# Performance work log

Measured on AMD Instinct MI355X. Metric: run time of the kernel, lower is better.

## Reference

```python
import jax, jax.numpy as jnp
import numpy as np

# Config (mirrors init_kwargs)
IN_FEATURES = 1024
N_CLASSES = 50257
CUTOFFS = [4000, 20000, 50257]   # cutoffs + [n_classes]
SHORTLIST = 4000
N_CLUSTERS = 2
HEAD_SIZE = SHORTLIST + N_CLUSTERS  # 4002
HSZ = [IN_FEATURES // 4, IN_FEATURES // 16]   # div_value**1, div_value**2 -> 256, 64
OSZ = [CUTOFFS[1] - CUTOFFS[0], CUTOFFS[2] - CUTOFFS[1]]  # 16000, 30257
N = 4096


def setup_inputs() -> dict:
    key = jax.random.key(0)
    ks = jax.random.split(key, 8)
    s = 0.02
    return {
        "myinput": jax.random.normal(ks[0], (N, IN_FEATURES), dtype=jnp.float32),
        "target": jax.random.randint(ks[1], (N,), 0, N_CLASSES),
        # head Linear (bias=False): weight stored as [in, out]
        "head_W": (jax.random.normal(ks[2], (IN_FEATURES, HEAD_SIZE), dtype=jnp.float32) * s),
        # tail cluster 0: Linear(in, 256, bias=False) -> Linear(256, 16000, bias=False)
        "t0_W1": (jax.random.normal(ks[3], (IN_FEATURES, HSZ[0]), dtype=jnp.float32) * s),
        "t0_W2": (jax.random.normal(ks[4], (HSZ[0], OSZ[0]), dtype=jnp.float32) * s),
        # tail cluster 1: Linear(in, 64, bias=False) -> Linear(64, 30257, bias=False)
        "t1_W1": (jax.random.normal(ks[5], (IN_FEATURES, HSZ[1]), dtype=jnp.float32) * s),
        "t1_W2": (jax.random.normal(ks[6], (HSZ[1], OSZ[1]), dtype=jnp.float32) * s),
    }


def _cluster_logprob(x, target, W1, W2, lo, hi, mask):
    # low-rank tail projection for one cluster, computed densely over all rows
    # then masked by membership (same math as the torch gather/scatter dispatch).
    logits = (x @ W1) @ W2                       # [N, osz]
    rel = jnp.clip(target - lo, 0, hi - lo - 1)  # in-range dummy for non-members
    picked = jnp.take_along_axis(logits, rel[:, None], axis=1)[:, 0]
    lp = picked - jax.nn.logsumexp(logits, axis=1)  # log_softmax gathered at rel
    return jnp.where(mask, lp, jnp.float32(0.0))


def reference(myinput, target, head_W, t0_W1, t0_W2, t1_W1, t1_W2):
    # Dropout (tail_drop) is identity in eval mode.
    in0 = (target >= CUTOFFS[0]) & (target < CUTOFFS[1])
    in1 = target >= CUTOFFS[1]
    # gather index into head: raw target for shortlist, cluster token otherwise
    gather_inds = jnp.where(in0, SHORTLIST, jnp.where(in1, SHORTLIST + 1, target))
    head_lp = jax.nn.log_softmax(myinput @ head_W, axis=-1)   # [N, 4002]
    out = jnp.take_along_axis(head_lp, gather_inds[:, None], axis=1)[:, 0]
    out = out + _cluster_logprob(myinput, target, t0_W1, t0_W2, CUTOFFS[0], CUTOFFS[1], in0)
    out = out + _cluster_logprob(myinput, target, t1_W1, t1_W2, CUTOFFS[1], CUTOFFS[2], in1)
    loss = -jnp.mean(out)
    return out, loss
```

## Files before the change

kernel.cpp:

```cpp
#include <hip/hip_runtime.h>
#include <hip/hip_bf16.h>
#include <math.h>
#include <stdint.h>

#define N_ROWS 4096
#define IN_F   1024
#define HEAD_N 4002
#define C0_H   256
#define C0_N   16000
#define C1_H   64
#define C1_N   30257
#define CUT0   4000
#define CUT1   20000
#define HW1    384

#define LOG2E 1.4426950408889634f
#define LN2   0.6931471805599453f

typedef __attribute__((ext_vector_type(8))) short bf16x8;
typedef __attribute__((ext_vector_type(4))) float f32x4;

__device__ __forceinline__ float exp2_fast(float x) {
    return __builtin_amdgcn_exp2f(x);
}

__device__ __forceinline__ ushort f2bf(float f) {
    uint32_t u = __builtin_bit_cast(uint32_t, f);
    uint32_t r = (u + 0x7fffu + ((u >> 16) & 1u)) >> 16;
    return (ushort)r;
}
__device__ __forceinline__ float bf2f(ushort u) {
    return __builtin_bit_cast(float, (uint32_t)u << 16);
}

__device__ __forceinline__ void gload_lds_16(const void* gsrc, void* ldst) {
    __builtin_amdgcn_global_load_lds(
        (const __attribute__((address_space(1))) void*)(uintptr_t)gsrc,
        (__attribute__((address_space(3))) void*)(uint32_t)(uintptr_t)ldst,
        16, 0, 0);
}

__global__ __launch_bounds__(256)
void cast_f32_bf16(const float* __restrict__ in, ushort* __restrict__ out, int n)
{
    int i = (blockIdx.x * 256 + threadIdx.x) * 4;
    if (i >= n) return;
    float4 v = *reinterpret_cast<const float4*>(in + i);
    ushort4 o;
    o.x = f2bf(v.x); o.y = f2bf(v.y); o.z = f2bf(v.z); o.w = f2bf(v.w);
    *reinterpret_cast<ushort4*>(out + i) = o;
}

__global__ __launch_bounds__(256)
void castT(const float* __restrict__ B, ushort* __restrict__ BT, int K, int N,
           float scale)
{
    __shared__ float t[32][33];
    const int tx = threadIdx.x, ty = threadIdx.y;
    const int n0 = blockIdx.x * 32, k0 = blockIdx.y * 32;
    #pragma unroll
    for (int i = 0; i < 4; ++i) {
        int n = n0 + tx;
        t[ty + i * 8][tx] = (n < N) ? B[(size_t)(k0 + ty + i * 8) * N + n] : 0.0f;
    }
    __syncthreads();
    #pragma unroll
    for (int i = 0; i < 4; ++i) {
        int n = n0 + ty + i * 8;
        BT[(size_t)n * K + k0 + tx] = f2bf(t[tx][ty + i * 8] * scale);
    }
}

__global__ __launch_bounds__(256)
void gemm_out(const ushort* __restrict__ A, int lda,
              const ushort* __restrict__ BT, int ldb, int K,
              int Nreal, ushort* __restrict__ Cout, int ldc)
{
    __shared__ ushort As[128 * 32];
    __shared__ ushort Bs[128 * 32];
    const int tid = threadIdx.x;
    const int l = tid & 63, w = tid >> 6;
    const int rowBase = blockIdx.y * 128, colBase = blockIdx.x * 128;
    const int rsel = l & 15, ksel = l >> 4;
    const int sr = l >> 2, skq = (l & 3) * 8;

    f32x4 acc[2][8];
    #pragma unroll
    for (int mi = 0; mi < 2; ++mi)
        #pragma unroll
        for (int ni = 0; ni < 8; ++ni) acc[mi][ni] = (f32x4){0.f, 0.f, 0.f, 0.f};

    for (int k0 = 0; k0 < K; k0 += 32) {
        #pragma unroll
        for (int i = 0; i < 2; ++i) {
            const int c = w + i * 4;
            gload_lds_16(A + (size_t)(rowBase + c * 16 + sr) * lda + k0 + skq,
                         (char*)As + c * 1024);
            gload_lds_16(BT + (size_t)(colBase + c * 16 + sr) * ldb + k0 + skq,
                         (char*)Bs + c * 1024);
        }
        __syncthreads();
        bf16x8 af[2], bfr[8];
        #pragma unroll
        for (int mi = 0; mi < 2; ++mi)
            af[mi] = *reinterpret_cast<const bf16x8*>(As + (w * 32 + mi * 16 + rsel) * 32 + ksel * 8);
        #pragma unroll
        for (int ni = 0; ni < 8; ++ni)
            bfr[ni] = *reinterpret_cast<const bf16x8*>(Bs + (ni * 16 + rsel) * 32 + ksel * 8);
        #pragma unroll
        for (int mi = 0; mi < 2; ++mi)
            #pragma unroll
            for (int ni = 0; ni < 8; ++ni)
                acc[mi][ni] = __builtin_amdgcn_mfma_f32_16x16x32_bf16(af[mi], bfr[ni], acc[mi][ni], 0, 0, 0);
        __syncthreads();
    }
    #pragma unroll
    for (int mi = 0; mi < 2; ++mi)
        #pragma unroll
        for (int ni = 0; ni < 8; ++ni) {
            const int col = colBase + ni * 16 + rsel;
            if (col < Nreal) {
                #pragma unroll
                for (int j = 0; j < 4; ++j) {
                    const int row = rowBase + w * 32 + mi * 16 + ksel * 4 + j;
                    Cout[(size_t)row * ldc + col] = f2bf(acc[mi][ni][j]);
                }
            }
        }
}

__global__ __launch_bounds__(256, 2)
void sumexp_pipe(const ushort* __restrict__ A, int lda,
                 const ushort* __restrict__ BT, int ldb,
                 int K, int nCT, int ntiles, int Nreal,
                 float* __restrict__ ps, int nsplit)
{
    __shared__ ushort As[2][128 * 32];
    __shared__ ushort Bs[2][256 * 32];
    __shared__ float sred[128];

    const int id = blockIdx.x;
    const int xsplit = ((id >> 8) << 3) + (id & 7);
    const int yrow   = (id & 255) >> 3;

    const int tid = threadIdx.x;
    const int l = tid & 63, w = tid >> 6;
    const int rowBase = yrow * 128;
    const int rsel = l & 15, ksel = l >> 4;

    const int kchunks = K >> 5;
    const int ct0 = xsplit * ntiles;
    const int ctn = min(ntiles, nCT - ct0);
    const int nch = ctn * kchunks;

    const int srow = l >> 2;
    const int skq = ((((l & 3) << 4) ^ ((srow & 3) << 4)) >> 1);

    const int wrow = (w >> 1) * 64;
    const int wcol = (w & 1) * 128;
    const int koff = (ksel * 8) ^ ((rsel & 3) << 3);

    f32x4 acc[4][8];
    float s_run[4][4];
    #pragma unroll
    for (int mi = 0; mi < 4; ++mi)
        #pragma unroll
        for (int j = 0; j < 4; ++j) s_run[mi][j] = 0.f;

    int i_kh = 0, i_ct = 0, issued = 0;
    #define ISSUE()                                                            \
    do {                                                                       \
        const int buf = issued & 1;                                            \
        const int k0 = i_kh << 5;                                              \
        const size_t cb = (size_t)(ct0 + i_ct) << 8;                           \
        _Pragma("unroll")                                                      \
        for (int i = 0; i < 2; ++i) {      \
            const int c = w * 2 + i;                                           \
            gload_lds_16(A + (size_t)(rowBase + c * 16 + srow) * lda + k0 + skq,\
                         (char*)&As[buf][0] + c * 1024);                       \
        }                                                                      \
        _Pragma("unroll")                                                      \
        for (int i = 0; i < 4; ++i) {    \
            const int c = w * 4 + i;                                           \
            gload_lds_16(BT + (cb + c * 16 + srow) * ldb + k0 + skq,           \
                         (char*)&Bs[buf][0] + c * 1024);                       \
        }                                                                      \
        ++issued;                                                              \
        if (++i_kh == kchunks) { i_kh = 0; ++i_ct; }                           \
    } while (0)

    ISSUE();
    if (nch > 1) ISSUE();

    int c_kh = 0;
    int c_colBase = ct0 << 8;

    for (int ch = 0; ch < nch; ++ch) {
        if (ch + 1 < nch) asm volatile("s_waitcnt vmcnt(6)" ::: "memory");
        else              asm volatile("s_waitcnt vmcnt(0)" ::: "memory");
        __builtin_amdgcn_s_barrier();

        if (c_kh == 0) {
            #pragma unroll
            for (int mi = 0; mi < 4; ++mi)
                #pragma unroll
                for (int ni = 0; ni < 8; ++ni)
                    acc[mi][ni] = (f32x4){0.f, 0.f, 0.f, 0.f};
        }

        const int buf = ch & 1;
        bf16x8 af[4], bfr[8];
        #pragma unroll
        for (int mi = 0; mi < 4; ++mi)
            af[mi] = *reinterpret_cast<const bf16x8*>(
                &As[buf][(wrow + mi * 16 + rsel) * 32 + koff]);
        #pragma unroll
        for (int ni = 0; ni < 8; ++ni)
            bfr[ni] = *reinterpret_cast<const bf16x8*>(
                &Bs[buf][(wcol + ni * 16 + rsel) * 32 + koff]);
        #pragma unroll
        for (int mi = 0; mi < 4; ++mi)
            #pragma unroll
            for (int ni = 0; ni < 8; ++ni)
                acc[mi][ni] = __builtin_amdgcn_mfma_f32_16x16x32_bf16(
                    af[mi], bfr[ni], acc[mi][ni], 0, 0, 0);

        __builtin_amdgcn_s_barrier();
        if (issued < nch) ISSUE();

        if (c_kh == kchunks - 1) {
            const int cbase = c_colBase + wcol;
            if (cbase + 128 > Nreal) {
                #pragma unroll
                for (int ni = 0; ni < 8; ++ni) {
                    const bool ok = (cbase + ni * 16 + rsel) < Nreal;
                    #pragma unroll
                    for (int mi = 0; mi < 4; ++mi)
                        #pragma unroll
                        for (int j = 0; j < 4; ++j)
                            s_run[mi][j] += ok ? exp2_fast(acc[mi][ni][j]) : 0.f;
                }
            } else {
                #pragma unroll
                for (int mi = 0; mi < 4; ++mi)
                    #pragma unroll
                    for (int ni = 0; ni < 8; ++ni)
                        #pragma unroll
                        for (int j = 0; j < 4; ++j)
                            s_run[mi][j] += exp2_fast(acc[mi][ni][j]);
            }
            c_kh = 0;
            c_colBase += 256;
        } else {
            ++c_kh;
        }
    }
    #undef ISSUE

    #pragma unroll
    for (int mi = 0; mi < 4; ++mi)
        #pragma unroll
        for (int j = 0; j < 4; ++j) {
            float S = s_run[mi][j];
            #pragma unroll
            for (int off = 8; off; off >>= 1) S += __shfl_xor(S, off);
            s_run[mi][j] = S;
            if ((w & 1) == 1 && rsel == 0)
                sred[wrow + mi * 16 + ksel * 4 + j] = S;
        }
    __syncthreads();
    if ((w & 1) == 0 && rsel == 0) {
        #pragma unroll
        for (int mi = 0; mi < 4; ++mi)
            #pragma unroll
            for (int j = 0; j < 4; ++j) {
                const int lrow = wrow + mi * 16 + ksel * 4 + j;
                ps[(size_t)(rowBase + lrow) * nsplit + xsplit] =
                    s_run[mi][j] + sred[lrow];
            }
    }
}

__global__ __launch_bounds__(256)
void gather_dot(const ushort* __restrict__ x_bf,
                const ushort* __restrict__ h_comb,
                const ushort* __restrict__ headWT,
                const ushort* __restrict__ t0W2T,
                const ushort* __restrict__ t1W2T,
                const int* __restrict__ target,
                float* __restrict__ pk_h, float* __restrict__ pk_c)
{
    const int r = blockIdx.x * 4 + (threadIdx.x >> 6);
    const int l = threadIdx.x & 63;
    const int t = target[r];

    const int gh = (t < CUT0) ? t : ((t < CUT1) ? CUT0 : CUT0 + 1);
    const ushort* xr = x_bf + (size_t)r * IN_F + l * 16;
    const ushort* wr = headWT + (size_t)gh * IN_F + l * 16;
    float s = 0.f;
    #pragma unroll
    for (int v = 0; v < 2; ++v) {
        ushort4 xa = *reinterpret_cast<const ushort4*>(xr + v * 8);
        ushort4 xb = *reinterpret_cast<const ushort4*>(xr + v * 8 + 4);
        ushort4 wa = *reinterpret_cast<const ushort4*>(wr + v * 8);
        ushort4 wb = *reinterpret_cast<const ushort4*>(wr + v * 8 + 4);
        s += bf2f(xa.x) * bf2f(wa.x) + bf2f(xa.y) * bf2f(wa.y)
           + bf2f(xa.z) * bf2f(wa.z) + bf2f(xa.w) * bf2f(wa.w)
           + bf2f(xb.x) * bf2f(wb.x) + bf2f(xb.y) * bf2f(wb.y)
           + bf2f(xb.z) * bf2f(wb.z) + bf2f(xb.w) * bf2f(wb.w);
    }
    #pragma unroll
    for (int off = 32; off; off >>= 1) s += __shfl_xor(s, off);
    if (l == 0) pk_h[r] = s * LN2;

    if (t >= CUT0) {
        float c = 0.f;
        if (t < CUT1) {
            const ushort* hr = h_comb + (size_t)r * HW1 + l * 4;
            const ushort* vr = t0W2T + (size_t)(t - CUT0) * C0_H + l * 4;
            ushort4 ha = *reinterpret_cast<const ushort4*>(hr);
            ushort4 va = *reinterpret_cast<const ushort4*>(vr);
            c = bf2f(ha.x) * bf2f(va.x) + bf2f(ha.y) * bf2f(va.y)
              + bf2f(ha.z) * bf2f(va.z) + bf2f(ha.w) * bf2f(va.w);
        } else {
            c = bf2f(h_comb[(size_t)r * HW1 + C0_H + l]) *
                bf2f(t1W2T[(size_t)(t - CUT1) * C1_H + l]);
        }
        #pragma unroll
        for (int off = 32; off; off >>= 1) c += __shfl_xor(c, off);
        if (l == 0) pk_c[r] = c * LN2;
    }
}

__global__ __launch_bounds__(256)
void combine_rows(const float* __restrict__ ps_h, const float* __restrict__ ps_0,
                  const float* __restrict__ ps_1,
                  const float* __restrict__ pk_h, const float* __restrict__ pk_c,
                  const int* __restrict__ target, float* __restrict__ out,
                  int ns_h, int ns_0, int ns_1)
{
    const int r = blockIdx.x * 256 + threadIdx.x;
    if (r >= N_ROWS) return;
    float S = 0.f;
    const float* p = ps_h + (size_t)r * ns_h;
    for (int i = 0; i < ns_h; ++i) S += p[i];
    float o = pk_h[r] - __logf(S);
    const int t = target[r];
    if (t >= CUT0) {
        const float* q; int n;
        if (t < CUT1) { q = ps_0 + (size_t)r * ns_0; n = ns_0; }
        else          { q = ps_1 + (size_t)r * ns_1; n = ns_1; }
        float S2 = 0.f;
        for (int i = 0; i < n; ++i) S2 += q[i];
        o += pk_c[r] - __logf(S2);
    }
    out[r] = o;
}

__global__ __launch_bounds__(256)
void finalize_loss(const float* __restrict__ out, float* __restrict__ loss)
{
    float s = 0.f;
    for (int r = threadIdx.x; r < N_ROWS; r += 256) s += out[r];
    #pragma unroll
    for (int off = 32; off; off >>= 1) s += __shfl_xor(s, off);
    __shared__ float red[4];
    if ((threadIdx.x & 63) == 0) red[threadIdx.x >> 6] = s;
    __syncthreads();
    if (threadIdx.x == 0)
        loss[0] = -(red[0] + red[1] + red[2] + red[3]) / (float)N_ROWS;
}

extern "C" void kernel_launch(void* const* d_in, const int* in_sizes, int n_in,
                              void* d_out, int out_size, void* d_ws, size_t ws_size,
                              hipStream_t stream)
{
    const float* x      = (const float*)d_in[0];
    const int*   target = (const int*)  d_in[1];
    const float* head_W = (const float*)d_in[2];
    const float* t0_W1  = (const float*)d_in[3];
    const float* t0_W2  = (const float*)d_in[4];
    const float* t1_W1  = (const float*)d_in[5];
    const float* t1_W2  = (const float*)d_in[6];
    float* out = (float*)d_out;

    const int HPAD  = 4096;
    const int C0PAD = 16128;
    const int C1PAD = 30464;
    const int nCT_h = HPAD / 256;
    const int nCT_0 = C0PAD / 256;
    const int nCT_1 = C1PAD / 256;

    const int NT_H = 2,  NS_H = 8;
    const int NT_0 = 4,  NS_0 = 16;
    const int NT_1 = 5,  NS_1 = 24;

    ushort* us = (ushort*)d_ws;
    ushort* x_bf   = us; us += (size_t)N_ROWS * IN_F;
    ushort* headWT = us; us += (size_t)HPAD * IN_F;
    ushort* hW1T   = us; us += (size_t)HW1 * IN_F;
    ushort* t0W2T  = us; us += (size_t)C0PAD * C0_H;
    ushort* t1W2T  = us; us += (size_t)C1PAD * C1_H;
    ushort* h_comb = us; us += (size_t)N_ROWS * HW1;

    float* ws   = (float*)us;
    float* ps_h = ws; ws += (size_t)N_ROWS * NS_H;
    float* ps_0 = ws; ws += (size_t)N_ROWS * NS_0;
    float* ps_1 = ws; ws += (size_t)N_ROWS * NS_1;
    float* pk_h = ws; ws += N_ROWS;
    float* pk_c = ws; ws += N_ROWS;

    const dim3 blk(256);

    hipLaunchKernelGGL(cast_f32_bf16, dim3(N_ROWS * IN_F / 1024), blk, 0, stream,
                       x, x_bf, N_ROWS * IN_F);
    hipLaunchKernelGGL(castT, dim3(HPAD / 32, IN_F / 32), dim3(32, 8), 0, stream,
                       head_W, headWT, IN_F, HEAD_N, LOG2E);
    hipLaunchKernelGGL(castT, dim3(C0_H / 32, IN_F / 32), dim3(32, 8), 0, stream,
                       t0_W1, hW1T, IN_F, C0_H, 1.0f);
    hipLaunchKernelGGL(castT, dim3(128 / 32, IN_F / 32), dim3(32, 8), 0, stream,
                       t1_W1, hW1T + (size_t)C0_H * IN_F, IN_F, C1_H, 1.0f);
    hipLaunchKernelGGL(castT, dim3(C0PAD / 32, C0_H / 32), dim3(32, 8), 0, stream,
                       t0_W2, t0W2T, C0_H, C0_N, LOG2E);
    hipLaunchKernelGGL(castT, dim3(C1PAD / 32, C1_H / 32), dim3(32, 8), 0, stream,
                       t1_W2, t1W2T, C1_H, C1_N, LOG2E);

    hipLaunchKernelGGL(gemm_out, dim3(HW1 / 128, N_ROWS / 128), blk, 0, stream,
                       x_bf, IN_F, hW1T, IN_F, IN_F, C0_H + C1_H, h_comb, HW1);

    hipLaunchKernelGGL(sumexp_pipe, dim3(NS_H * 32), blk, 0, stream,
                       x_bf, IN_F, headWT, IN_F, IN_F, nCT_h, NT_H, HEAD_N, ps_h, NS_H);
    hipLaunchKernelGGL(sumexp_pipe, dim3(NS_0 * 32), blk, 0, stream,
                       h_comb, HW1, t0W2T, C0_H, C0_H, nCT_0, NT_0, C0_N, ps_0, NS_0);
    hipLaunchKernelGGL(sumexp_pipe, dim3(NS_1 * 32), blk, 0, stream,
                       h_comb + C0_H, HW1, t1W2T, C1_H, C1_H, nCT_1, NT_1, C1_N, ps_1, NS_1);

    hipLaunchKernelGGL(gather_dot, dim3(N_ROWS / 4), blk, 0, stream,
                       x_bf, h_comb, headWT, t0W2T, t1W2T, target, pk_h, pk_c);
    hipLaunchKernelGGL(combine_rows, dim3(N_ROWS / 256), blk, 0, stream,
                       ps_h, ps_0, ps_1, pk_h, pk_c, target, out, NS_H, NS_0, NS_1);
    hipLaunchKernelGGL(finalize_loss, dim3(1), blk, 0, stream, out, out + N_ROWS);
}
```

Before: 197.1 us.

## Reshape sumexp tiles to 256 rows by 128 cols and drop cross-wave reduction

The fused GEMM+sum-exp kernel now uses a 256x128 block tile instead of 128x256. Each wave owns 64 full rows across all 128 columns, so per-row partial sums come straight from a shuffle reduction and the LDS cross-wave reduction and its barrier go away. Split counts and tiles per split are retuned, occupancy is raised to 3 blocks per SM, and blocks with no work are guarded. In exchange, every wave re-reads the whole B tile from LDS, and the extra splits enlarge the partial-sum buffer that combine_rows must reduce.

```diff
diff --git a/kernel.cpp b/kernel.cpp
--- a/kernel.cpp
+++ b/kernel.cpp
@@ -129,35 +129,32 @@
         }
 }
 
-__global__ __launch_bounds__(256, 2)
+__global__ __launch_bounds__(256, 3)
 void sumexp_pipe(const ushort* __restrict__ A, int lda,
                  const ushort* __restrict__ BT, int ldb,
                  int K, int nCT, int ntiles, int Nreal,
                  float* __restrict__ ps, int nsplit)
 {
-    __shared__ ushort As[2][128 * 32];
-    __shared__ ushort Bs[2][256 * 32];
-    __shared__ float sred[128];
+    __shared__ ushort As[2][256 * 32];
+    __shared__ ushort Bs[2][128 * 32];
 
     const int id = blockIdx.x;
-    const int xsplit = ((id >> 8) << 3) + (id & 7);
-    const int yrow   = (id & 255) >> 3;
+    const int xsplit = ((id >> 7) << 3) + (id & 7);
+    const int yrow   = (id >> 3) & 15;
 
     const int tid = threadIdx.x;
     const int l = tid & 63, w = tid >> 6;
-    const int rowBase = yrow * 128;
+    const int rowBase = yrow * 256;
     const int rsel = l & 15, ksel = l >> 4;
 
     const int kchunks = K >> 5;
     const int ct0 = xsplit * ntiles;
     const int ctn = min(ntiles, nCT - ct0);
-    const int nch = ctn * kchunks;
+    const int nch = (ctn > 0) ? ctn * kchunks : 0;
 
     const int srow = l >> 2;
     const int skq = ((((l & 3) << 4) ^ ((srow & 3) << 4)) >> 1);
 
-    const int wrow = (w >> 1) * 64;
-    const int wcol = (w & 1) * 128;
     const int koff = (ksel * 8) ^ ((rsel & 3) << 3);
 
     f32x4 acc[4][8];
@@ -172,16 +169,16 @@
     do {                                                                       \
         const int buf = issued & 1;                                            \
         const int k0 = i_kh << 5;                                              \
-        const size_t cb = (size_t)(ct0 + i_ct) << 8;                           \
+        const size_t cb = (size_t)(ct0 + i_ct) << 7;                           \
         _Pragma("unroll")                                                      \
-        for (int i = 0; i < 2; ++i) {      \
-            const int c = w * 2 + i;                                           \
+        for (int i = 0; i < 4; ++i) {    \
+            const int c = w * 4 + i;                                           \
             gload_lds_16(A + (size_t)(rowBase + c * 16 + srow) * lda + k0 + skq,\
                          (char*)&As[buf][0] + c * 1024);                       \
         }                                                                      \
         _Pragma("unroll")                                                      \
-        for (int i = 0; i < 4; ++i) {    \
-            const int c = w * 4 + i;                                           \
+        for (int i = 0; i < 2; ++i) {      \
+            const int c = w * 2 + i;                                           \
             gload_lds_16(BT + (cb + c * 16 + srow) * ldb + k0 + skq,           \
                          (char*)&Bs[buf][0] + c * 1024);                       \
         }                                                                      \
@@ -189,70 +186,71 @@
         if (++i_kh == kchunks) { i_kh = 0; ++i_ct; }                           \
     } while (0)
 
-    ISSUE();
-    if (nch > 1) ISSUE();
-
-    int c_kh = 0;
-    int c_colBase = ct0 << 8;
-
-    for (int ch = 0; ch < nch; ++ch) {
-        if (ch + 1 < nch) asm volatile("s_waitcnt vmcnt(6)" ::: "memory");
-        else              asm volatile("s_waitcnt vmcnt(0)" ::: "memory");
-        __builtin_amdgcn_s_barrier();
-
-        if (c_kh == 0) {
+    if (nch > 0) {
+        ISSUE();
+        if (nch > 1) ISSUE();
+
+        int c_kh = 0;
+        int c_colBase = ct0 << 7;
+
+        for (int ch = 0; ch < nch; ++ch) {
+            if (ch + 1 < nch) asm volatile("s_waitcnt vmcnt(6)" ::: "memory");
+            else              asm volatile("s_waitcnt vmcnt(0)" ::: "memory");
+            __builtin_amdgcn_s_barrier();
+
+            if (c_kh == 0) {
+                #pragma unroll
+                for (int mi = 0; mi < 4; ++mi)
+                    #pragma unroll
+                    for (int ni = 0; ni < 8; ++ni)
+                        acc[mi][ni] = (f32x4){0.f, 0.f, 0.f, 0.f};
+            }
+
+            const int buf = ch & 1;
+            bf16x8 af[4], bfr[8];
+            #pragma unroll
+            for (int mi = 0; mi < 4; ++mi)
+                af[mi] = *reinterpret_cast<const bf16x8*>(
+                    &As[buf][(w * 64 + mi * 16 + rsel) * 32 + koff]);
+            #pragma unroll
+            for (int ni = 0; ni < 8; ++ni)
+                bfr[ni] = *reinterpret_cast<const bf16x8*>(
+                    &Bs[buf][(ni * 16 + rsel) * 32 + koff]);
             #pragma unroll
             for (int mi = 0; mi < 4; ++mi)
                 #pragma unroll
                 for (int ni = 0; ni < 8; ++ni)
-                    acc[mi][ni] = (f32x4){0.f, 0.f, 0.f, 0.f};
-        }
-
-        const int buf = ch & 1;
-        bf16x8 af[4], bfr[8];
-        #pragma unroll
-        for (int mi = 0; mi < 4; ++mi)
-            af[mi] = *reinterpret_cast<const bf16x8*>(
-                &As[buf][(wrow + mi * 16 + rsel) * 32 + koff]);
-        #pragma unroll
-        for (int ni = 0; ni < 8; ++ni)
-            bfr[ni] = *reinterpret_cast<const bf16x8*>(
-                &Bs[buf][(wcol + ni * 16 + rsel) * 32 + koff]);
-        #pragma unroll
-        for (int mi = 0; mi < 4; ++mi)
-            #pragma unroll
-            for (int ni = 0; ni < 8; ++ni)
-                acc[mi][ni] = __builtin_amdgcn_mfma_f32_16x16x32_bf16(
-                    af[mi], bfr[ni], acc[mi][ni], 0, 0, 0);
-
-        __builtin_amdgcn_s_barrier();
-        if (issued < nch) ISSUE();
-
-        if (c_kh == kchunks - 1) {
-            const int cbase = c_colBase + wcol;
-            if (cbase + 128 > Nreal) {
-                #pragma unroll
-                for (int ni = 0; ni < 8; ++ni) {
-                    const bool ok = (cbase + ni * 16 + rsel) < Nreal;
+                    acc[mi][ni] = __builtin_amdgcn_mfma_f32_16x16x32_bf16(
+                        af[mi], bfr[ni], acc[mi][ni], 0, 0, 0);
+
+            __builtin_amdgcn_s_barrier();
+            if (issued < nch) ISSUE();
+
+            if (c_kh == kchunks - 1) {
+                if (c_colBase + 128 > Nreal) {
+                    #pragma unroll
+                    for (int ni = 0; ni < 8; ++ni) {
+                        const bool ok = (c_colBase + ni * 16 + rsel) < Nreal;
+                        #pragma unroll
+                        for (int mi = 0; mi < 4; ++mi)
+                            #pragma unroll
+                            for (int j = 0; j < 4; ++j)
+                                s_run[mi][j] += ok ? exp2_fast(acc[mi][ni][j]) : 0.f;
+                    }
+                } else {
                     #pragma unroll
                     for (int mi = 0; mi < 4; ++mi)
                         #pragma unroll
-                        for (int j = 0; j < 4; ++j)
-                            s_run[mi][j] += ok ? exp2_fast(acc[mi][ni][j]) : 0.f;
+                        for (int ni = 0; ni < 8; ++ni)
+                            #pragma unroll
+                            for (int j = 0; j < 4; ++j)
+                                s_run[mi][j] += exp2_fast(acc[mi][ni][j]);
                 }
+                c_kh = 0;
+                c_colBase += 128;
             } else {
-                #pragma unroll
-                for (int mi = 0; mi < 4; ++mi)
-                    #pragma unroll
-                    for (int ni = 0; ni < 8; ++ni)
-                        #pragma unroll
-                        for (int j = 0; j < 4; ++j)
-                            s_run[mi][j] += exp2_fast(acc[mi][ni][j]);
+                ++c_kh;
             }
-            c_kh = 0;
-            c_colBase += 256;
-        } else {
-            ++c_kh;
         }
     }
     #undef ISSUE
@@ -264,21 +262,11 @@
             float S = s_run[mi][j];
             #pragma unroll
             for (int off = 8; off; off >>= 1) S += __shfl_xor(S, off);
-            s_run[mi][j] = S;
-            if ((w & 1) == 1 && rsel == 0)
-                sred[wrow + mi * 16 + ksel * 4 + j] = S;
+            if (rsel == 0) {
+                const int row = rowBase + w * 64 + mi * 16 + ksel * 4 + j;
+                ps[(size_t)row * nsplit + xsplit] = S;
+            }
         }
-    __syncthreads();
-    if ((w & 1) == 0 && rsel == 0) {
-        #pragma unroll
-        for (int mi = 0; mi < 4; ++mi)
-            #pragma unroll
-            for (int j = 0; j < 4; ++j) {
-                const int lrow = wrow + mi * 16 + ksel * 4 + j;
-                ps[(size_t)(rowBase + lrow) * nsplit + xsplit] =
-                    s_run[mi][j] + sred[lrow];
-            }
-    }
 }
 
 __global__ __launch_bounds__(256)
@@ -387,13 +375,13 @@
     const int HPAD  = 4096;
     const int C0PAD = 16128;
     const int C1PAD = 30464;
-    const int nCT_h = HPAD / 256;
-    const int nCT_0 = C0PAD / 256;
-    const int nCT_1 = C1PAD / 256;
-
-    const int NT_H = 2,  NS_H = 8;
-    const int NT_0 = 4,  NS_0 = 16;
-    const int NT_1 = 5,  NS_1 = 24;
+    const int nCT_h = HPAD / 128;
+    const int nCT_0 = C0PAD / 128;
+    const int nCT_1 = C1PAD / 128;
+
+    const int NT_H = 2,  NS_H = 16;
+    const int NT_0 = 3,  NS_0 = 48;
+    const int NT_1 = 5,  NS_1 = 48;
 
     ushort* us = (ushort*)d_ws;
     ushort* x_bf   = us; us += (size_t)N_ROWS * IN_F;
@@ -428,11 +416,11 @@
     hipLaunchKernelGGL(gemm_out, dim3(HW1 / 128, N_ROWS / 128), blk, 0, stream,
                        x_bf, IN_F, hW1T, IN_F, IN_F, C0_H + C1_H, h_comb, HW1);
 
-    hipLaunchKernelGGL(sumexp_pipe, dim3(NS_H * 32), blk, 0, stream,
+    hipLaunchKernelGGL(sumexp_pipe, dim3(NS_H * 16), blk, 0, stream,
                        x_bf, IN_F, headWT, IN_F, IN_F, nCT_h, NT_H, HEAD_N, ps_h, NS_H);
-    hipLaunchKernelGGL(sumexp_pipe, dim3(NS_0 * 32), blk, 0, stream,
+    hipLaunchKernelGGL(sumexp_pipe, dim3(NS_0 * 16), blk, 0, stream,
                        h_comb, HW1, t0W2T, C0_H, C0_H, nCT_0, NT_0, C0_N, ps_0, NS_0);
-    hipLaunchKernelGGL(sumexp_pipe, dim3(NS_1 * 32), blk, 0, stream,
+    hipLaunchKernelGGL(sumexp_pipe, dim3(NS_1 * 16), blk, 0, stream,
                        h_comb + C0_H, HW1, t1W2T, C1_H, C1_H, nCT_1, NT_1, C1_N, ps_1, NS_1);
 
     hipLaunchKernelGGL(gather_dot, dim3(N_ROWS / 4), blk, 0, stream,
```

Measured after the change: 555.0 us. 182% more time.
